# Optimization experiments

Hardware: AMD Instinct MI355X
Metric: run time of the kernel (lower is better)

The kernel has to match this reference:

```python
import jax, jax.numpy as jnp
import numpy as np

SEQ_LEN = 200
BATCH = 32768
H = 4  # LSTM hidden size


def _lstm_layer(x, Wih, Whh, bih, bhh):
    """PyTorch-semantics LSTM layer. x: [B,T,D] -> [B,T,H]. Gate order i,f,g,o."""
    # precompute input contribution for all timesteps: [B,T,4H]
    xg = jnp.einsum('btd,gd->btg', x, Wih) + bih + bhh

    def step(carry, xt):
        h, c = carry
        g = xt + h @ Whh.T  # [B,4H]
        i, f, gg, o = jnp.split(g, 4, axis=-1)
        c = jax.nn.sigmoid(f) * c + jax.nn.sigmoid(i) * jnp.tanh(gg)
        h = jax.nn.sigmoid(o) * jnp.tanh(c)
        return (h, c), h

    B = x.shape[0]
    z = jnp.zeros((B, Whh.shape[1]), x.dtype)
    _, hs = jax.lax.scan(step, (z, z), jnp.swapaxes(xg, 0, 1))  # [T,B,H]
    return jnp.swapaxes(hs, 0, 1)


def _lstm2(x, Wih0, Whh0, bih0, bhh0, Wih1, Whh1, bih1, bhh1):
    h = _lstm_layer(x, Wih0, Whh0, bih0, bhh0)
    return _lstm_layer(h, Wih1, Whh1, bih1, bhh1)


def setup_inputs() -> dict:
    key = jax.random.key(0)
    ks = iter(jax.random.split(key, 64))
    def p(shape, s=0.1):
        return jax.random.normal(next(ks), shape, jnp.float32) * s
    d = {"x": jax.random.normal(next(ks), (BATCH, 2, SEQ_LEN), jnp.float32)}
    for r in ("r0", "r1"):
        d[f"{r}_Wih0"] = p((4 * H, 1)); d[f"{r}_Whh0"] = p((4 * H, H))
        d[f"{r}_bih0"] = p((4 * H,));  d[f"{r}_bhh0"] = p((4 * H,))
        d[f"{r}_Wih1"] = p((4 * H, H)); d[f"{r}_Whh1"] = p((4 * H, H))
        d[f"{r}_bih1"] = p((4 * H,));  d[f"{r}_bhh1"] = p((4 * H,))
    d["Wp"] = p((40, 2 * SEQ_LEN)); d["bp"] = p((40,))
    d["WH"] = p((128, 4 * SEQ_LEN)); d["bH"] = p((128,))
    d["WL"] = p((128, 4 * SEQ_LEN)); d["bL"] = p((128,))
    d["W1"] = p((80, 256)); d["b1"] = p((80,))
    d["W2"] = p((40, 80)); d["b2"] = p((40,))
    d["W3"] = p((1, 80)); d["b3"] = p((1,))
    return d


def reference(x,
              r0_Wih0, r0_Whh0, r0_bih0, r0_bhh0, r0_Wih1, r0_Whh1, r0_bih1, r0_bhh1,
              r1_Wih0, r1_Whh0, r1_bih0, r1_bhh0, r1_Wih1, r1_Whh1, r1_bih1, r1_bhh1,
              Wp, bp, WH, bH, WL, bL, W1, b1, W2, b2, W3, b3):
    B = x.shape[0]
    x_flat = x.reshape(B, 2 * SEQ_LEN)
    other = x_flat @ Wp.T + bp  # [B,40]

    Hx = x[:, 0, :, None]  # [B,T,1]
    Lx = x[:, 1, :, None]
    Hh = _lstm2(Hx, r0_Wih0, r0_Whh0, r0_bih0, r0_bhh0, r0_Wih1, r0_Whh1, r0_bih1, r0_bhh1)
    Lh = _lstm2(Lx, r1_Wih0, r1_Whh0, r1_bih0, r1_bhh0, r1_Wih1, r1_Whh1, r1_bih1, r1_bhh1)
    Hf = jnp.tanh(Hh.reshape(B, 4 * SEQ_LEN) @ WH.T + bH)  # [B,128]
    Lf = jnp.tanh(Lh.reshape(B, 4 * SEQ_LEN) @ WL.T + bL)
    z = jnp.concatenate([Hf, Lf], axis=1)  # [B,256]
    z = jnp.tanh(z @ W1.T + b1)  # [B,80]
    z = jnp.tanh(z @ W2.T + b2)  # [B,40]
    z = jnp.concatenate([z, other], axis=1)  # [B,80]
    return jax.nn.sigmoid(z @ W3.T + b3)  # [B,1]
```

## Files before the change

kernel.cpp:

```cpp
#include <hip/hip_runtime.h>
#include <hip/hip_bf16.h>

#define BATCH 32768
#define TSEQ 200

typedef __attribute__((ext_vector_type(8))) short short8;
typedef __attribute__((ext_vector_type(4))) float floatx4;
typedef __attribute__((ext_vector_type(2))) float f32x2;

#if __has_builtin(__builtin_amdgcn_exp2f)
__device__ __forceinline__ float EXP2(float x) { return __builtin_amdgcn_exp2f(x); }
#else
__device__ __forceinline__ float EXP2(float x) {
    float r; asm("v_exp_f32 %0, %1" : "=v"(r) : "v"(x)); return r;
}
#endif
__device__ __forceinline__ float RCP(float x) { return __builtin_amdgcn_rcpf(x); }

__device__ __forceinline__ float fast_sigmoid(float x) {
    return RCP(1.0f + EXP2(-1.4426950408889634f * x));
}
__device__ __forceinline__ float fast_tanh(float x) {
    float e = EXP2(2.8853900817779268f * x);
    return 1.0f - 2.0f * RCP(e + 1.0f);
}
__device__ __forceinline__ short f2bfs(float v) {
    __hip_bfloat16 h = __float2bfloat16(v);
    return __builtin_bit_cast(short, h);
}
__device__ __forceinline__ f32x2 splat2(float x) { f32x2 v; v[0] = x; v[1] = x; return v; }
__device__ __forceinline__ f32x2 pkfma(f32x2 a, f32x2 b, f32x2 c) {
    return __builtin_elementwise_fma(a, b, c);
}
template <int K>
__device__ __forceinline__ float qb(float v) {
    int i = __builtin_bit_cast(int, v);
    int r = __builtin_amdgcn_update_dpp(i, i, K * 0x55, 0xf, 0xf, false);
    return __builtin_bit_cast(float, r);
}
__device__ __forceinline__ void async16(void* lds, const void* g) {
    __builtin_amdgcn_global_load_lds(
        (const __attribute__((address_space(1))) unsigned int*)g,
        (__attribute__((address_space(3))) unsigned int*)lds, 16, 0, 0);
}

#define S_SIG (-1.4426950408889634f)
#define S_TANH (2.8853900817779268f)

#define WS_HH  0
#define WS_WHB 104857600
#define WS_WLB (WS_WHB + 204800)
#define WS_W1B (WS_WLB + 204800)
#define WS_W2B (WS_W1B + 40960)
#define WS_U   (WS_W2B + 9216)

struct LW { const float* p[16]; };

__global__ __launch_bounds__(256) void k_prep(
    const float* __restrict__ WH, const float* __restrict__ WL,
    const float* __restrict__ W1, const float* __restrict__ W2,
    const float* __restrict__ W3, const float* __restrict__ Wp,
    const float* __restrict__ bp, const float* __restrict__ b3,
    __hip_bfloat16* __restrict__ WHbf, __hip_bfloat16* __restrict__ WLbf,
    __hip_bfloat16* __restrict__ W1bf, __hip_bfloat16* __restrict__ W2bf,
    float* __restrict__ u)
{
    int gid = blockIdx.x * 256 + threadIdx.x;
    int n = gid / 800, k = gid - n * 800;
    int t = k >> 2, q = k & 3;
    int kp = (t >> 2) * 16 + q * 4 + (t & 3);
    int dst = n * 800 + kp;
    WHbf[dst] = __float2bfloat16(WH[gid]);
    WLbf[dst] = __float2bfloat16(WL[gid]);
    if (gid < 20480) W1bf[gid] = __float2bfloat16(W1[gid]);
    if (gid < 4608) {
        int rr = gid / 96, cc = gid - rr * 96;
        float v = (rr < 40 && cc < 80) ? W2[rr * 80 + cc] : 0.0f;
        W2bf[gid] = __float2bfloat16(v);
    }
    if (gid < 400) {
        float a = 0.f;
        for (int j = 0; j < 40; ++j) a = fmaf(W3[40 + j], Wp[j * 400 + gid], a);
        u[gid] = a;
    } else if (gid == 400) {
        float a = b3[0];
        for (int j = 0; j < 40; ++j) a = fmaf(W3[40 + j], bp[j], a);
        u[400] = a;
    }
}

template <int M>
__device__ __forceinline__ float lstm_round(
    float xt, float& h0, float& c0, float& h1, float& c1,
    const f32x2 (&wx0p)[2], const f32x2 (&bb0p)[2], const f32x2 (&whh0p)[2][4],
    const f32x2 (&bb1p)[2], const f32x2 (&wih1p)[2][4], const f32x2 (&whh1p)[2][4])
{
    float a0 = qb<0>(h0), a1 = qb<1>(h0), a2 = qb<2>(h0), a3 = qb<3>(h0);
    float h1out = 0.f;

    if (M != 1) {
        float q0 = qb<0>(h1), q1 = qb<1>(h1), q2 = qb<2>(h1), q3 = qb<3>(h1);
        f32x2 G0 = bb1p[0], G1 = bb1p[1];
        G0 = pkfma(wih1p[0][0], splat2(a0), G0); G1 = pkfma(wih1p[1][0], splat2(a0), G1);
        G0 = pkfma(wih1p[0][1], splat2(a1), G0); G1 = pkfma(wih1p[1][1], splat2(a1), G1);
        G0 = pkfma(wih1p[0][2], splat2(a2), G0); G1 = pkfma(wih1p[1][2], splat2(a2), G1);
        G0 = pkfma(wih1p[0][3], splat2(a3), G0); G1 = pkfma(wih1p[1][3], splat2(a3), G1);
        G0 = pkfma(whh1p[0][0], splat2(q0), G0); G1 = pkfma(whh1p[1][0], splat2(q0), G1);
        G0 = pkfma(whh1p[0][1], splat2(q1), G0); G1 = pkfma(whh1p[1][1], splat2(q1), G1);
        G0 = pkfma(whh1p[0][2], splat2(q2), G0); G1 = pkfma(whh1p[1][2], splat2(q2), G1);
        G0 = pkfma(whh1p[0][3], splat2(q3), G0); G1 = pkfma(whh1p[1][3], splat2(q3), G1);
        float ig = RCP(1.0f + EXP2(G0[0]));
        float fg = RCP(1.0f + EXP2(G0[1]));
        float og = RCP(1.0f + EXP2(G1[1]));
        float tg = 1.0f - 2.0f * RCP(EXP2(G1[0]) + 1.0f);
        c1 = fmaf(fg, c1, ig * tg);
        float th1 = 1.0f - 2.0f * RCP(EXP2(S_TANH * c1) + 1.0f);
        h1 = og * th1;
        h1out = h1;
    }

    if (M != 2) {
        f32x2 g0 = pkfma(splat2(xt), wx0p[0], bb0p[0]);
        f32x2 g1 = pkfma(splat2(xt), wx0p[1], bb0p[1]);
        g0 = pkfma(whh0p[0][0], splat2(a0), g0); g1 = pkfma(whh0p[1][0], splat2(a0), g1);
        g0 = pkfma(whh0p[0][1], splat2(a1), g0); g1 = pkfma(whh0p[1][1], splat2(a1), g1);
        g0 = pkfma(whh0p[0][2], splat2(a2), g0); g1 = pkfma(whh0p[1][2], splat2(a2), g1);
        g0 = pkfma(whh0p[0][3], splat2(a3), g0); g1 = pkfma(whh0p[1][3], splat2(a3), g1);
        float ig = RCP(1.0f + EXP2(g0[0]));
        float fg = RCP(1.0f + EXP2(g0[1]));
        float og = RCP(1.0f + EXP2(g1[1]));
        float tg = 1.0f - 2.0f * RCP(EXP2(g1[0]) + 1.0f);
        c0 = fmaf(fg, c0, ig * tg);
        float th0 = 1.0f - 2.0f * RCP(EXP2(S_TANH * c0) + 1.0f);
        h0 = og * th0;
    }
    return h1out;
}

__global__ __launch_bounds__(256)
__attribute__((amdgpu_waves_per_eu(4, 4))) void k_fused(
    const float* __restrict__ x, LW w, const float* __restrict__ u,
    __hip_bfloat16* __restrict__ hh,
    const __hip_bfloat16* __restrict__ WHbf, const __hip_bfloat16* __restrict__ WLbf,
    const float* __restrict__ bH, const float* __restrict__ bL,
    const __hip_bfloat16* __restrict__ W1bf, const __hip_bfloat16* __restrict__ W2bf,
    const float* __restrict__ b1, const float* __restrict__ b2,
    const float* __restrict__ W3, float* __restrict__ out)
{
    __shared__ __align__(16) char smem[33024];
    short* Bse = (short*)smem;
    short* zl  = (short*)smem;
    short* z1l = (short*)(smem + 17024);
    float* z2l = (float*)(smem + 23808);
    float* ot  = (float*)(smem + 32768);

    int tid = threadIdx.x;
    int q = tid & 3;
    int g = tid >> 2;
    int r = tid >> 7;
    int b = blockIdx.x * 32 + (g & 31);

    const float* Wih0 = w.p[r * 8 + 0];
    const float* Whh0 = w.p[r * 8 + 1];
    const float* bih0 = w.p[r * 8 + 2];
    const float* bhh0 = w.p[r * 8 + 3];
    const float* Wih1 = w.p[r * 8 + 4];
    const float* Whh1 = w.p[r * 8 + 5];
    const float* bih1 = w.p[r * 8 + 6];
    const float* bhh1 = w.p[r * 8 + 7];

    f32x2 wx0p[2], bb0p[2], bb1p[2], whh0p[2][4], wih1p[2][4], whh1p[2][4];
#pragma unroll
    for (int p = 0; p < 2; ++p) {
#pragma unroll
        for (int c = 0; c < 2; ++c) {
            int G = 2 * p + c;
            int j = 4 * G + q;
            float sc = (G == 2) ? S_TANH : S_SIG;
            wx0p[p][c] = Wih0[j] * sc;
            bb0p[p][c] = (bih0[j] + bhh0[j]) * sc;
            bb1p[p][c] = (bih1[j] + bhh1[j]) * sc;
#pragma unroll
            for (int k = 0; k < 4; ++k) {
                whh0p[p][k][c] = Whh0[j * 4 + k] * sc;
                wih1p[p][k][c] = Wih1[j * 4 + k] * sc;
                whh1p[p][k][c] = Whh1[j * 4 + k] * sc;
            }
        }
    }

    const float* xp = x + ((size_t)b * 2 + r) * TSEQ;
    const float* up = u + r * TSEQ;
    __hip_bfloat16* hp = hh + ((size_t)r * BATCH + b) * 800 + q * 4;

    float h0 = 0.f, c0 = 0.f, h1 = 0.f, c1 = 0.f, accO = 0.f;

    float4 xv_prev = *(const float4*)xp;
    float4 uv_prev = *(const float4*)up;

    accO = fmaf(xv_prev.x, uv_prev.x, accO);
    lstm_round<1>(xv_prev.x, h0, c0, h1, c1,
                  wx0p, bb0p, whh0p, bb1p, wih1p, whh1p);

    for (int tb = 0; tb <= 192; tb += 4) {
        float4 xv_new = *(const float4*)(xp + tb + 4);
        float4 uv_new = *(const float4*)(up + tb + 4);
        float xc[4] = {xv_prev.y, xv_prev.z, xv_prev.w, xv_new.x};
        float uc[4] = {uv_prev.y, uv_prev.z, uv_prev.w, uv_new.x};
        float hb[4];
#pragma unroll
        for (int j = 0; j < 4; ++j) {
            accO = fmaf(xc[j], uc[j], accO);
            hb[j] = lstm_round<0>(xc[j], h0, c0, h1, c1,
                                  wx0p, bb0p, whh0p, bb1p, wih1p, whh1p);
        }
        ushort4 pk;
        pk.x = (unsigned short)f2bfs(hb[0]);
        pk.y = (unsigned short)f2bfs(hb[1]);
        pk.z = (unsigned short)f2bfs(hb[2]);
        pk.w = (unsigned short)f2bfs(hb[3]);
        *(ushort4*)(hp + tb * 4) = pk;
        xv_prev = xv_new; uv_prev = uv_new;
    }

    {
        float xc[3] = {xv_prev.y, xv_prev.z, xv_prev.w};
        float uc[3] = {uv_prev.y, uv_prev.z, uv_prev.w};
        float hb[4];
#pragma unroll
        for (int j = 0; j < 3; ++j) {
            accO = fmaf(xc[j], uc[j], accO);
            hb[j] = lstm_round<0>(xc[j], h0, c0, h1, c1,
                                  wx0p, bb0p, whh0p, bb1p, wih1p, whh1p);
        }
        hb[3] = lstm_round<2>(0.f, h0, c0, h1, c1,
                              wx0p, bb0p, whh0p, bb1p, wih1p, whh1p);
        ushort4 pk;
        pk.x = (unsigned short)f2bfs(hb[0]);
        pk.y = (unsigned short)f2bfs(hb[1]);
        pk.z = (unsigned short)f2bfs(hb[2]);
        pk.w = (unsigned short)f2bfs(hb[3]);
        *(ushort4*)(hp + 196 * 4) = pk;
    }
    if (q == 0) ot[g] = accO;
    __syncthreads();

    int wv = tid >> 6, lane = tid & 63, l15 = lane & 15, quad = lane >> 4;
    int b0 = blockIdx.x * 32;
    int f = wv >> 1, mt = wv & 1;

    const __hip_bfloat16* gB0 = WHbf + (size_t)(wv * 16 + (tid & 15)) * 800 + ((tid >> 4) & 3) * 8;
    const __hip_bfloat16* gB2 = WLbf + (size_t)(wv * 16 + (tid & 15)) * 800 + ((tid >> 4) & 3) * 8;
    const __hip_bfloat16* Ab =
        hh + ((size_t)f * BATCH + b0 + mt * 16 + l15) * 800 + quad * 8;

#define PF(kc, buf)                                                    \
    do {                                                               \
        char* lb_ = smem + (buf) * 16384 + wv * 1024;                  \
        async16(lb_,          gB0 + (kc) * 32);                        \
        async16(lb_ + 4096,   gB0 + 64 * 800 + (kc) * 32);             \
        async16(lb_ + 8192,   gB2 + (kc) * 32);                        \
        async16(lb_ + 12288,  gB2 + 64 * 800 + (kc) * 32);             \
    } while (0)

    floatx4 acc[8] = {};
    short8 af = *(const short8*)(const void*)Ab;
    PF(0, 0);
    for (int kc = 0; kc < 25; ++kc) {
        __syncthreads();
        short8 afn = af;
        if (kc < 24) {
            PF(kc + 1, (kc + 1) & 1);
            afn = *(const short8*)(const void*)(Ab + (kc + 1) * 32);
        }
        const short* Bb = Bse + (kc & 1) * 8192 + f * 4096 + lane * 8;
#pragma unroll
        for (int nt = 0; nt < 8; ++nt) {
            short8 bfr = *(const short8*)(const void*)(Bb + nt * 512);
            acc[nt] = __builtin_amdgcn_mfma_f32_16x16x32_bf16(af, bfr, acc[nt], 0, 0, 0);
        }
        af = afn;
    }
#undef PF
    __syncthreads();

    {
        const float* bias = f ? bL : bH;
#pragma unroll
        for (int nt = 0; nt < 8; ++nt) {
            float bb = bias[nt * 16 + l15];
            int c = f * 128 + nt * 16 + l15;
#pragma unroll
            for (int rg = 0; rg < 4; ++rg) {
                int m = mt * 16 + quad * 4 + rg;
                zl[m * 264 + c] = f2bfs(fast_tanh(acc[nt][rg] + bb));
            }
        }
    }
    __syncthreads();

    if (wv < 2) {
        floatx4 a1[5] = {};
        for (int kc = 0; kc < 8; ++kc) {
            short8 afz = *(const short8*)(const void*)
                &zl[(wv * 16 + l15) * 264 + kc * 32 + quad * 8];
#pragma unroll
            for (int nt = 0; nt < 5; ++nt) {
                short8 bfr = *(const short8*)(const void*)
                    (W1bf + (size_t)(nt * 16 + l15) * 256 + kc * 32 + quad * 8);
                a1[nt] = __builtin_amdgcn_mfma_f32_16x16x32_bf16(afz, bfr, a1[nt], 0, 0, 0);
            }
        }
#pragma unroll
        for (int nt = 0; nt < 5; ++nt) {
            int n = nt * 16 + l15;
            float bb = b1[n];
#pragma unroll
            for (int rg = 0; rg < 4; ++rg)
                z1l[(wv * 16 + quad * 4 + rg) * 104 + n] = f2bfs(fast_tanh(a1[nt][rg] + bb));
        }
    } else {
        int i0 = tid - 128;
        for (int i = i0; i < 512; i += 128) {
            int rr = i >> 4, cc = 80 + (i & 15);
            z1l[rr * 104 + cc] = 0;
        }
    }
    __syncthreads();

    if (wv < 2) {
        floatx4 a2[3] = {};
        for (int kc = 0; kc < 3; ++kc) {
            short8 afz = *(const short8*)(const void*)
                &z1l[(wv * 16 + l15) * 104 + kc * 32 + quad * 8];
#pragma unroll
            for (int nt = 0; nt < 3; ++nt) {
                short8 bfr = *(const short8*)(const void*)
                    (W2bf + (size_t)(nt * 16 + l15) * 96 + kc * 32 + quad * 8);
                a2[nt] = __builtin_amdgcn_mfma_f32_16x16x32_bf16(afz, bfr, a2[nt], 0, 0, 0);
            }
        }
#pragma unroll
        for (int nt = 0; nt < 3; ++nt) {
            int n = nt * 16 + l15;
            if (n < 40) {
                float bb = b2[n];
#pragma unroll
                for (int rg = 0; rg < 4; ++rg)
                    z2l[(wv * 16 + quad * 4 + rg) * 44 + n] = fast_tanh(a2[nt][rg] + bb);
            }
        }
    }
    __syncthreads();

    if (tid < 32) {
        float s = u[400] + ot[tid] + ot[32 + tid];
        for (int j = 0; j < 40; ++j) s = fmaf(z2l[tid * 44 + j], W3[j], s);
        out[b0 + tid] = fast_sigmoid(s);
    }
}

extern "C" void kernel_launch(void* const* d_in, const int* in_sizes, int n_in,
                              void* d_out, int out_size, void* d_ws, size_t ws_size,
                              hipStream_t stream)
{
    const float* x = (const float*)d_in[0];
    LW w;
    for (int i = 0; i < 16; ++i) w.p[i] = (const float*)d_in[1 + i];
    const float* Wp = (const float*)d_in[17];
    const float* bp = (const float*)d_in[18];
    const float* WH = (const float*)d_in[19];
    const float* bH = (const float*)d_in[20];
    const float* WL = (const float*)d_in[21];
    const float* bL = (const float*)d_in[22];
    const float* W1 = (const float*)d_in[23];
    const float* b1 = (const float*)d_in[24];
    const float* W2 = (const float*)d_in[25];
    const float* b2 = (const float*)d_in[26];
    const float* W3 = (const float*)d_in[27];
    const float* b3 = (const float*)d_in[28];

    char* ws = (char*)d_ws;
    __hip_bfloat16* hh   = (__hip_bfloat16*)(ws + WS_HH);
    __hip_bfloat16* WHbf = (__hip_bfloat16*)(ws + WS_WHB);
    __hip_bfloat16* WLbf = (__hip_bfloat16*)(ws + WS_WLB);
    __hip_bfloat16* W1bf = (__hip_bfloat16*)(ws + WS_W1B);
    __hip_bfloat16* W2bf = (__hip_bfloat16*)(ws + WS_W2B);
    float* u = (float*)(ws + WS_U);
    float* out = (float*)d_out;

    k_prep<<<400, 256, 0, stream>>>(WH, WL, W1, W2, W3, Wp, bp, b3,
                                    WHbf, WLbf, W1bf, W2bf, u);
    k_fused<<<1024, 256, 0, stream>>>(x, w, u, hh, WHbf, WLbf, bH, bL,
                                      W1bf, W2bf, b1, b2, W3, out);
}
```

Baseline: 308.2 us.

## Fold weight-prep kernel into fused kernel with on-the-fly bf16 conversion

Removes the separate k_prep launch. Each block now computes the collapsed Wp·W3 vector u in LDS and converts the fp32 WH/WL/W1/W2 weights to bf16 in registers as it loads them. The async global→LDS prefetch of pre-converted bf16 B tiles becomes register loads of fp32 data plus packed-convert writes into LDS. This saves one launch and a workspace round trip, but every block redoes the conversion, reads twice the weight bytes, and adds a u computation of about 400×40 FMAs with strided Wp reads before the LSTM starts.

```diff
diff --git a/kernel.cpp b/kernel.cpp
--- a/kernel.cpp
+++ b/kernel.cpp
@@ -28,6 +28,9 @@
     __hip_bfloat16 h = __float2bfloat16(v);
     return __builtin_bit_cast(short, h);
 }
+__device__ __forceinline__ int cvtpk(float lo, float hi) {
+    int r; asm("v_cvt_pk_bf16_f32 %0, %1, %2" : "=v"(r) : "v"(lo), "v"(hi)); return r;
+}
 __device__ __forceinline__ f32x2 splat2(float x) { f32x2 v; v[0] = x; v[1] = x; return v; }
 __device__ __forceinline__ f32x2 pkfma(f32x2 a, f32x2 b, f32x2 c) {
     return __builtin_elementwise_fma(a, b, c);
@@ -38,56 +41,11 @@
     int r = __builtin_amdgcn_update_dpp(i, i, K * 0x55, 0xf, 0xf, false);
     return __builtin_bit_cast(float, r);
 }
-__device__ __forceinline__ void async16(void* lds, const void* g) {
-    __builtin_amdgcn_global_load_lds(
-        (const __attribute__((address_space(1))) unsigned int*)g,
-        (__attribute__((address_space(3))) unsigned int*)lds, 16, 0, 0);
-}
 
 #define S_SIG (-1.4426950408889634f)
 #define S_TANH (2.8853900817779268f)
 
-#define WS_HH  0
-#define WS_WHB 104857600
-#define WS_WLB (WS_WHB + 204800)
-#define WS_W1B (WS_WLB + 204800)
-#define WS_W2B (WS_W1B + 40960)
-#define WS_U   (WS_W2B + 9216)
-
 struct LW { const float* p[16]; };
-
-__global__ __launch_bounds__(256) void k_prep(
-    const float* __restrict__ WH, const float* __restrict__ WL,
-    const float* __restrict__ W1, const float* __restrict__ W2,
-    const float* __restrict__ W3, const float* __restrict__ Wp,
-    const float* __restrict__ bp, const float* __restrict__ b3,
-    __hip_bfloat16* __restrict__ WHbf, __hip_bfloat16* __restrict__ WLbf,
-    __hip_bfloat16* __restrict__ W1bf, __hip_bfloat16* __restrict__ W2bf,
-    float* __restrict__ u)
-{
-    int gid = blockIdx.x * 256 + threadIdx.x;
-    int n = gid / 800, k = gid - n * 800;
-    int t = k >> 2, q = k & 3;
-    int kp = (t >> 2) * 16 + q * 4 + (t & 3);
-    int dst = n * 800 + kp;
-    WHbf[dst] = __float2bfloat16(WH[gid]);
-    WLbf[dst] = __float2bfloat16(WL[gid]);
-    if (gid < 20480) W1bf[gid] = __float2bfloat16(W1[gid]);
-    if (gid < 4608) {
-        int rr = gid / 96, cc = gid - rr * 96;
-        float v = (rr < 40 && cc < 80) ? W2[rr * 80 + cc] : 0.0f;
-        W2bf[gid] = __float2bfloat16(v);
-    }
-    if (gid < 400) {
-        float a = 0.f;
-        for (int j = 0; j < 40; ++j) a = fmaf(W3[40 + j], Wp[j * 400 + gid], a);
-        u[gid] = a;
-    } else if (gid == 400) {
-        float a = b3[0];
-        for (int j = 0; j < 40; ++j) a = fmaf(W3[40 + j], bp[j], a);
-        u[400] = a;
-    }
-}
 
 template <int M>
 __device__ __forceinline__ float lstm_round(
@@ -139,22 +97,45 @@
 
 __global__ __launch_bounds__(256)
 __attribute__((amdgpu_waves_per_eu(4, 4))) void k_fused(
-    const float* __restrict__ x, LW w, const float* __restrict__ u,
+    const float* __restrict__ x, LW w,
+    const float* __restrict__ Wp, const float* __restrict__ bp,
+    const float* __restrict__ b3, const float* __restrict__ W3,
     __hip_bfloat16* __restrict__ hh,
-    const __hip_bfloat16* __restrict__ WHbf, const __hip_bfloat16* __restrict__ WLbf,
+    const float* __restrict__ WHf, const float* __restrict__ WLf,
     const float* __restrict__ bH, const float* __restrict__ bL,
-    const __hip_bfloat16* __restrict__ W1bf, const __hip_bfloat16* __restrict__ W2bf,
+    const float* __restrict__ W1f, const float* __restrict__ W2f,
     const float* __restrict__ b1, const float* __restrict__ b2,
-    const float* __restrict__ W3, float* __restrict__ out)
+    float* __restrict__ out)
 {
-    __shared__ __align__(16) char smem[33024];
+    __shared__ __align__(16) char smem[33040];
+    float* u_lds = (float*)smem;
     short* Bse = (short*)smem;
     short* zl  = (short*)smem;
     short* z1l = (short*)(smem + 17024);
     float* z2l = (float*)(smem + 23808);
     float* ot  = (float*)(smem + 32768);
+    float* u400s = (float*)(smem + 33024);
 
     int tid = threadIdx.x;
+
+    {
+        float a = 0.f;
+        for (int j = 0; j < 40; ++j) a = fmaf(W3[40 + j], Wp[j * 400 + tid], a);
+        u_lds[tid] = a;
+        if (tid < 144) {
+            int g2 = tid + 256;
+            float a2 = 0.f;
+            for (int j = 0; j < 40; ++j) a2 = fmaf(W3[40 + j], Wp[j * 400 + g2], a2);
+            u_lds[g2] = a2;
+        }
+        if (tid == 0) {
+            float a3 = b3[0];
+            for (int j = 0; j < 40; ++j) a3 = fmaf(W3[40 + j], bp[j], a3);
+            *u400s = a3;
+        }
+    }
+    __syncthreads();
+
     int q = tid & 3;
     int g = tid >> 2;
     int r = tid >> 7;
@@ -190,7 +171,7 @@
     }
 
     const float* xp = x + ((size_t)b * 2 + r) * TSEQ;
-    const float* up = u + r * TSEQ;
+    const float* up = u_lds + r * TSEQ;
     __hip_bfloat16* hp = hh + ((size_t)r * BATCH + b) * 800 + q * 4;
 
     float h0 = 0.f, c0 = 0.f, h1 = 0.f, c1 = 0.f, accO = 0.f;
@@ -249,28 +230,51 @@
     int b0 = blockIdx.x * 32;
     int f = wv >> 1, mt = wv & 1;
 
-    const __hip_bfloat16* gB0 = WHbf + (size_t)(wv * 16 + (tid & 15)) * 800 + ((tid >> 4) & 3) * 8;
-    const __hip_bfloat16* gB2 = WLbf + (size_t)(wv * 16 + (tid & 15)) * 800 + ((tid >> 4) & 3) * 8;
+    int qd = lane >> 4;
+    const float* Wsrc = (qd < 2) ? WHf : WLf;
+    int wrow = (qd & 1) * 64 + wv * 16 + l15;
+    const float* wsp = Wsrc + (size_t)wrow * 800;
+    char* ldsb = smem + qd * 4096 + wv * 1024 + l15 * 16;
+
+    float4 va0, va1, va2, va3, vb0, vb1, vb2, vb3;
+
+#define EPLOAD(kc)                                                     \
+    do { const float* s_ = wsp + (kc) * 32;                            \
+         va0 = *(const float4*)(s_);                                   \
+         va1 = *(const float4*)(s_ + 4);                               \
+         va2 = *(const float4*)(s_ + 8);                               \
+         va3 = *(const float4*)(s_ + 12);                              \
+         vb0 = *(const float4*)(s_ + 16);                              \
+         vb1 = *(const float4*)(s_ + 20);                              \
+         vb2 = *(const float4*)(s_ + 24);                              \
+         vb3 = *(const float4*)(s_ + 28); } while (0)
+
+#define EPWRITE(buf)                                                   \
+    do { char* d_ = ldsb + (buf) * 16384;                              \
+         int4 t0, t1;                                                  \
+         t0.x = cvtpk(va0.x, va1.x); t0.y = cvtpk(va2.x, va3.x);       \
+         t0.z = cvtpk(va0.y, va1.y); t0.w = cvtpk(va2.y, va3.y);       \
+         t1.x = cvtpk(va0.z, va1.z); t1.y = cvtpk(va2.z, va3.z);       \
+         t1.z = cvtpk(va0.w, va1.w); t1.w = cvtpk(va2.w, va3.w);       \
+         *(int4*)(d_) = t0; *(int4*)(d_ + 256) = t1;                   \
+         t0.x = cvtpk(vb0.x, vb1.x); t0.y = cvtpk(vb2.x, vb3.x);       \
+         t0.z = cvtpk(vb0.y, vb1.y); t0.w = cvtpk(vb2.y, vb3.y);       \
+         t1.x = cvtpk(vb0.z, vb1.z); t1.y = cvtpk(vb2.z, vb3.z);       \
+         t1.z = cvtpk(vb0.w, vb1.w); t1.w = cvtpk(vb2.w, vb3.w);       \
+         *(int4*)(d_ + 512) = t0; *(int4*)(d_ + 768) = t1;             \
+    } while (0)
+
     const __hip_bfloat16* Ab =
         hh + ((size_t)f * BATCH + b0 + mt * 16 + l15) * 800 + quad * 8;
 
-#define PF(kc, buf)                                                    \
-    do {                                                               \
-        char* lb_ = smem + (buf) * 16384 + wv * 1024;                  \
-        async16(lb_,          gB0 + (kc) * 32);                        \
-        async16(lb_ + 4096,   gB0 + 64 * 800 + (kc) * 32);             \
-        async16(lb_ + 8192,   gB2 + (kc) * 32);                        \
-        async16(lb_ + 12288,  gB2 + 64 * 800 + (kc) * 32);             \
-    } while (0)
-
     floatx4 acc[8] = {};
+    EPLOAD(0); EPWRITE(0);
     short8 af = *(const short8*)(const void*)Ab;
-    PF(0, 0);
     for (int kc = 0; kc < 25; ++kc) {
         __syncthreads();
         short8 afn = af;
         if (kc < 24) {
-            PF(kc + 1, (kc + 1) & 1);
+            EPLOAD(kc + 1);
             afn = *(const short8*)(const void*)(Ab + (kc + 1) * 32);
         }
         const short* Bb = Bse + (kc & 1) * 8192 + f * 4096 + lane * 8;
@@ -279,9 +283,11 @@
             short8 bfr = *(const short8*)(const void*)(Bb + nt * 512);
             acc[nt] = __builtin_amdgcn_mfma_f32_16x16x32_bf16(af, bfr, acc[nt], 0, 0, 0);
         }
+        if (kc < 24) EPWRITE((kc + 1) & 1);
         af = afn;
     }
-#undef PF
+#undef EPLOAD
+#undef EPWRITE
     __syncthreads();
 
     {
@@ -306,8 +312,13 @@
                 &zl[(wv * 16 + l15) * 264 + kc * 32 + quad * 8];
 #pragma unroll
             for (int nt = 0; nt < 5; ++nt) {
-                short8 bfr = *(const short8*)(const void*)
-                    (W1bf + (size_t)(nt * 16 + l15) * 256 + kc * 32 + quad * 8);
+                const float* ws1 = W1f + (size_t)(nt * 16 + l15) * 256 + kc * 32 + quad * 8;
+                float4 wa = *(const float4*)ws1;
+                float4 wb = *(const float4*)(ws1 + 4);
+                int4 wi;
+                wi.x = cvtpk(wa.x, wa.y); wi.y = cvtpk(wa.z, wa.w);
+                wi.z = cvtpk(wb.x, wb.y); wi.w = cvtpk(wb.z, wb.w);
+                short8 bfr = __builtin_bit_cast(short8, wi);
                 a1[nt] = __builtin_amdgcn_mfma_f32_16x16x32_bf16(afz, bfr, a1[nt], 0, 0, 0);
             }
         }
@@ -331,12 +342,21 @@
     if (wv < 2) {
         floatx4 a2[3] = {};
         for (int kc = 0; kc < 3; ++kc) {
-            short8 afz = *(const short8*)(const void*)
-                &z1l[(wv * 16 + l15) * 104 + kc * 32 + quad * 8];
 #pragma unroll
             for (int nt = 0; nt < 3; ++nt) {
-                short8 bfr = *(const short8*)(const void*)
-                    (W2bf + (size_t)(nt * 16 + l15) * 96 + kc * 32 + quad * 8);
+                short8 afz = *(const short8*)(const void*)
+                    &z1l[(wv * 16 + l15) * 104 + kc * 32 + quad * 8];
+                bool valid = ((nt < 2) || (l15 < 8)) && ((kc < 2) || (quad < 2));
+                short8 bfr = {};
+                if (valid) {
+                    const float* ws2 = W2f + (size_t)(nt * 16 + l15) * 80 + kc * 32 + quad * 8;
+                    float4 wa = *(const float4*)ws2;
+                    float4 wb = *(const float4*)(ws2 + 4);
+                    int4 wi;
+                    wi.x = cvtpk(wa.x, wa.y); wi.y = cvtpk(wa.z, wa.w);
+                    wi.z = cvtpk(wb.x, wb.y); wi.w = cvtpk(wb.z, wb.w);
+                    bfr = __builtin_bit_cast(short8, wi);
+                }
                 a2[nt] = __builtin_amdgcn_mfma_f32_16x16x32_bf16(afz, bfr, a2[nt], 0, 0, 0);
             }
         }
@@ -354,7 +374,7 @@
     __syncthreads();
 
     if (tid < 32) {
-        float s = u[400] + ot[tid] + ot[32 + tid];
+        float s = *u400s + ot[tid] + ot[32 + tid];
         for (int j = 0; j < 40; ++j) s = fmaf(z2l[tid * 44 + j], W3[j], s);
         out[b0 + tid] = fast_sigmoid(s);
     }
@@ -380,17 +400,9 @@
     const float* W3 = (const float*)d_in[27];
     const float* b3 = (const float*)d_in[28];
 
-    char* ws = (char*)d_ws;
-    __hip_bfloat16* hh   = (__hip_bfloat16*)(ws + WS_HH);
-    __hip_bfloat16* WHbf = (__hip_bfloat16*)(ws + WS_WHB);
-    __hip_bfloat16* WLbf = (__hip_bfloat16*)(ws + WS_WLB);
-    __hip_bfloat16* W1bf = (__hip_bfloat16*)(ws + WS_W1B);
-    __hip_bfloat16* W2bf = (__hip_bfloat16*)(ws + WS_W2B);
-    float* u = (float*)(ws + WS_U);
+    __hip_bfloat16* hh = (__hip_bfloat16*)d_ws;
     float* out = (float*)d_out;
 
-    k_prep<<<400, 256, 0, stream>>>(WH, WL, W1, W2, W3, Wp, bp, b3,
-                                    WHbf, WLbf, W1bf, W2bf, u);
-    k_fused<<<1024, 256, 0, stream>>>(x, w, u, hh, WHbf, WLbf, bH, bL,
-                                      W1bf, W2bf, b1, b2, W3, out);
-}
+    k_fused<<<1024, 256, 0, stream>>>(x, w, Wp, bp, b3, W3, hh,
+                                      WH, WL, bH, bL, W1, W2, b1, b2, out);
+}
```

New measurement: 353.2 us. 1.15x slower.
